# Performance work log

Measured on AMD Instinct MI355X. Metric: run time of the kernel, lower is better.

## Reference

```python
import jax, jax.numpy as jnp
import numpy as np

L = 2048; V = 50000; E = 256
H1 = 512; H2 = 512; H3 = 512; H4 = 512
T = 11; START = 9; STOP = 10; ALPHA = 0.2
NEG = -10000.0


def setup_inputs() -> dict:
    key = jax.random.key(0)
    ks = jax.random.split(key, 25)
    def n(k, shape, s=0.05):
        return jax.random.normal(k, shape, dtype=jnp.float32) * s
    h1 = H1 // 2; h2 = H4 // 2
    trans = jax.random.normal(ks[23], (T, T), dtype=jnp.float32)
    trans = trans.at[START, :].set(NEG).at[:, STOP].set(NEG)
    return {
        "sentence": jax.random.randint(ks[0], (L,), 0, V),
        "emb": n(ks[1], (V, E), 0.1),
        "l1_wih_f": n(ks[2], (4 * h1, E)), "l1_whh_f": n(ks[3], (4 * h1, h1)), "l1_b_f": n(ks[4], (4 * h1,)),
        "l1_wih_b": n(ks[5], (4 * h1, E)), "l1_whh_b": n(ks[6], (4 * h1, h1)), "l1_b_b": n(ks[7], (4 * h1,)),
        "hc1": n(ks[8], (4, h1)),
        "gat1_W": n(ks[9], (H1, H2)), "gat1_a": n(ks[10], (2 * H2,)),
        "gat2_W": n(ks[11], (H2, H3)), "gat2_a": n(ks[12], (2 * H3,)),
        "l2_wih_f": n(ks[13], (4 * h2, H3)), "l2_whh_f": n(ks[14], (4 * h2, h2)), "l2_b_f": n(ks[15], (4 * h2,)),
        "l2_wih_b": n(ks[16], (4 * h2, H3)), "l2_whh_b": n(ks[17], (4 * h2, h2)), "l2_b_b": n(ks[18], (4 * h2,)),
        "hc2": n(ks[19], (4, h2)),
        "w_tag": n(ks[20], (T, H4)), "b_tag": n(ks[21], (T,)),
        "trans": trans,
    }


def _lstm_dir(x, h0, c0, wih, whh, b):
    # x: [L, D]; PyTorch gate order i, f, g, o
    def step(carry, xt):
        h, c = carry
        z = xt @ wih.T + h @ whh.T + b
        i, f, g, o = jnp.split(z, 4)
        i = jax.nn.sigmoid(i); f = jax.nn.sigmoid(f)
        g = jnp.tanh(g); o = jax.nn.sigmoid(o)
        c = f * c + i * g
        h = o * jnp.tanh(c)
        return (h, c), h
    _, hs = jax.lax.scan(step, (h0, c0), x)
    return hs


def _bilstm(x, wf, uf, bf, wb, ub, bb, hc):
    hf = _lstm_dir(x, hc[0], hc[1], wf, uf, bf)
    hb = _lstm_dir(x[::-1], hc[2], hc[3], wb, ub, bb)[::-1]
    return jnp.concatenate([hf, hb], axis=-1)  # [L, 2h]


def _gat(h, W, a):
    # dense GAT layer: attention over all node pairs (inference, no dropout)
    Wh = h @ W                                   # [L, F]
    F = W.shape[1]
    e = jax.nn.leaky_relu((Wh @ a[:F])[:, None] + (Wh @ a[F:])[None, :], ALPHA)  # [L, L]
    attn = jax.nn.softmax(e, axis=1)
    return attn @ Wh


def _viterbi(feats, trans):
    init = jnp.full((T,), NEG, dtype=feats.dtype).at[START].set(0.0)
    def step(fv, feat):
        scores = fv[None, :] + trans             # [next_tag, prev_tag]
        bp = jnp.argmax(scores, axis=1)
        fv2 = jnp.max(scores, axis=1) + feat
        return fv2, bp
    fv, bps = jax.lax.scan(step, init, feats)    # bps: [L, T]
    term = fv + trans[STOP]
    best = jnp.argmax(term)
    score = term[best]
    def back(tag, bp):
        return bp[tag], tag
    _, path = jax.lax.scan(back, best, bps, reverse=True)
    return score, path


def reference(sentence, emb, l1_wih_f, l1_whh_f, l1_b_f, l1_wih_b, l1_whh_b, l1_b_b, hc1,
              gat1_W, gat1_a, gat2_W, gat2_a,
              l2_wih_f, l2_whh_f, l2_b_f, l2_wih_b, l2_whh_b, l2_b_b, hc2,
              w_tag, b_tag, trans):
    x = emb[sentence]                                                  # [L, E]
    h1 = _bilstm(x, l1_wih_f, l1_whh_f, l1_b_f, l1_wih_b, l1_whh_b, l1_b_b, hc1)
    g1 = jax.nn.elu(_gat(h1, gat1_W, gat1_a))
    g2 = jax.nn.elu(_gat(g1, gat2_W, gat2_a))
    h2 = _bilstm(g2, l2_wih_f, l2_whh_f, l2_b_f, l2_wih_b, l2_whh_b, l2_b_b, hc2)
    feats = h2 @ w_tag.T + b_tag                                       # [L, T]
    score, path = _viterbi(feats, trans)
    return score, path
```

## Files before the change

kernel.cpp:

```cpp
#include <hip/hip_runtime.h>
#include <hip/hip_bf16.h>
#include <math.h>

#define SEQL 2048
#define EDIM 256
#define HID 256
#define G4 1024
#define HCAT 512
#define TT 11
#define START_TAG 9
#define STOP_TAG 10
#define NEGV -10000.0f
#define ALPHA_LR 0.2f
#define VCH 64
#define VCS 32
#define NU 16
#define NBLK 16

__device__ __forceinline__ float sigf(float x) { return 1.0f / (1.0f + __expf(-x)); }
__device__ __forceinline__ float tanhfast(float x) { return 2.0f / (1.0f + __expf(-2.0f * x)) - 1.0f; }
__device__ __forceinline__ unsigned int bfp(float f) {
    union { float f; unsigned int u; } c; c.f = f;
    return (c.u + 0x7FFFu + ((c.u >> 16) & 1u)) >> 16;
}
__device__ __forceinline__ float bflo(unsigned int u) { return __uint_as_float(u << 16); }
__device__ __forceinline__ float bfhi(unsigned int u) { return __uint_as_float(u & 0xFFFF0000u); }

__global__ void embed_k(const int* __restrict__ sent, const float* __restrict__ emb,
                        float* __restrict__ x) {
    int idx = blockIdx.x * 256 + threadIdx.x;
    int t = idx >> 8, e = idx & 255;
    x[idx] = emb[(size_t)sent[t] * EDIM + e];
}

__global__ __launch_bounds__(256) void gemm_nt(const float* __restrict__ A,
                                               const float* __restrict__ B,
                                               const float* __restrict__ bias,
                                               float* __restrict__ C,
                                               int M, int N, int K) {
    __shared__ float As[16][68];
    __shared__ float Bs[16][68];
    int tid = threadIdx.x;
    int tx = tid & 15, ty = tid >> 4;
    int m0 = blockIdx.y * 64, n0 = blockIdx.x * 64;
    int lr = tid >> 2;
    int lc = (tid & 3) * 4;
    float acc[4][4] = {};
    for (int k0 = 0; k0 < K; k0 += 16) {
        float4 av = *(const float4*)(A + (size_t)(m0 + lr) * K + k0 + lc);
        float4 bv = make_float4(0.f, 0.f, 0.f, 0.f);
        if (n0 + lr < N) bv = *(const float4*)(B + (size_t)(n0 + lr) * K + k0 + lc);
        As[lc + 0][lr] = av.x; As[lc + 1][lr] = av.y; As[lc + 2][lr] = av.z; As[lc + 3][lr] = av.w;
        Bs[lc + 0][lr] = bv.x; Bs[lc + 1][lr] = bv.y; Bs[lc + 2][lr] = bv.z; Bs[lc + 3][lr] = bv.w;
        __syncthreads();
#pragma unroll
        for (int kk = 0; kk < 16; ++kk) {
            float4 a4 = *(const float4*)&As[kk][ty * 4];
            float4 b4 = *(const float4*)&Bs[kk][tx * 4];
            float aa[4] = {a4.x, a4.y, a4.z, a4.w};
            float bb[4] = {b4.x, b4.y, b4.z, b4.w};
#pragma unroll
            for (int i = 0; i < 4; ++i)
#pragma unroll
                for (int j = 0; j < 4; ++j) acc[i][j] += aa[i] * bb[j];
        }
        __syncthreads();
    }
#pragma unroll
    for (int i = 0; i < 4; ++i) {
        int m = m0 + ty * 4 + i;
#pragma unroll
        for (int j = 0; j < 4; ++j) {
            int n = n0 + tx * 4 + j;
            if (n < N) {
                float v = acc[i][j];
                if (bias) v += bias[n];
                C[(size_t)m * N + n] = v;
            }
        }
    }
}

__global__ __launch_bounds__(256) void gemm_nn_ks(const float* __restrict__ A,
                                                  const float* __restrict__ B,
                                                  float* __restrict__ Cpart,
                                                  int M, int N, int K4) {
    __shared__ float As[16][68];
    __shared__ float Bs[16][68];
    int tid = threadIdx.x;
    int tx = tid & 15, ty = tid >> 4;
    int m0 = blockIdx.y * 64, n0 = blockIdx.x * 64;
    int kz = blockIdx.z;
    int K = (int)gridDim.z * K4;
    int kbeg = kz * K4, kend = kbeg + K4;
    int lr = tid >> 2;
    int lc = (tid & 3) * 4;
    int br = tid >> 4;
    int bc = (tid & 15) * 4;
    float acc[4][4] = {};
    for (int k0 = kbeg; k0 < kend; k0 += 16) {
        float4 av = *(const float4*)(A + (size_t)(m0 + lr) * K + k0 + lc);
        float4 bv = *(const float4*)(B + (size_t)(k0 + br) * N + n0 + bc);
        As[lc + 0][lr] = av.x; As[lc + 1][lr] = av.y; As[lc + 2][lr] = av.z; As[lc + 3][lr] = av.w;
        *(float4*)&Bs[br][bc] = bv;
        __syncthreads();
#pragma unroll
        for (int kk = 0; kk < 16; ++kk) {
            float4 a4 = *(const float4*)&As[kk][ty * 4];
            float4 b4 = *(const float4*)&Bs[kk][tx * 4];
            float aa[4] = {a4.x, a4.y, a4.z, a4.w};
            float bb[4] = {b4.x, b4.y, b4.z, b4.w};
#pragma unroll
            for (int i = 0; i < 4; ++i)
#pragma unroll
                for (int j = 0; j < 4; ++j) acc[i][j] += aa[i] * bb[j];
        }
        __syncthreads();
    }
    float* Cz = Cpart + (size_t)kz * M * N;
#pragma unroll
    for (int i = 0; i < 4; ++i) {
        int m = m0 + ty * 4 + i;
#pragma unroll
        for (int j = 0; j < 4; ++j) {
            int n = n0 + tx * 4 + j;
            Cz[(size_t)m * N + n] = acc[i][j];
        }
    }
}

__global__ void attn_fin(const float* __restrict__ Cp, const float* __restrict__ Zr,
                         float* __restrict__ C, int MN, int N) {
    int idx = blockIdx.x * 256 + threadIdx.x;
    float v = Cp[idx] + Cp[MN + idx] + Cp[2 * MN + idx] + Cp[3 * MN + idx];
    v /= Zr[idx / N];
    C[idx] = v > 0.f ? v : (__expf(v) - 1.f);
}

__global__ void sum4_fin(const float* __restrict__ Cp, float* __restrict__ C, int MN) {
    int idx = blockIdx.x * 256 + threadIdx.x;
    C[idx] = Cp[idx] + Cp[MN + idx] + Cp[2 * MN + idx] + Cp[3 * MN + idx];
}

__global__ __launch_bounds__(256) void lstm_lds(const float* __restrict__ xin_f,
                                                const float* __restrict__ xin_b,
                                                const float* __restrict__ whh_f,
                                                const float* __restrict__ whh_b,
                                                const float* __restrict__ hc,
                                                float* __restrict__ out,
                                                unsigned int* pubu, int tagbase) {
    int raw = blockIdx.x;
    int lane7 = raw & 7;
    if (lane7 > 1) return;
    int dir = lane7;
    int b = raw >> 3;
    const float* xin = dir ? xin_b : xin_f;
    const float* whh = dir ? whh_b : whh_f;

    int tid = threadIdx.x;

    __shared__ uint4 W4[2048];
    __shared__ __align__(16) float hbuf[256];
    __shared__ float zp[512];

    for (int idx = tid; idx < 2048; idx += 256) {
        int wave = idx >> 9;
        int i = (idx >> 6) & 7;
        int l = idx & 63;
        int towner = wave * 64 + l;
        int rp = towner & 31;
        int k8 = towner >> 5;
        int rloc = 2 * rp + (i >> 2);
        int ii = i & 3;
        int g = rloc >> 4, j = rloc & 15;
        const float* wr = whh + (size_t)(g * HID + b * NU + j) * HID + k8 * 32 + ii * 8;
        uint4 v;
        v.x = bfp(wr[0]) | (bfp(wr[1]) << 16);
        v.y = bfp(wr[2]) | (bfp(wr[3]) << 16);
        v.z = bfp(wr[4]) | (bfp(wr[5]) << 16);
        v.w = bfp(wr[6]) | (bfp(wr[7]) << 16);
        W4[wave * 512 + i * 64 + l] = v;
    }

    if (tid < 256) hbuf[tid] = hc[dir * 512 + tid];
    float c = 0.f;
    float xq0 = 0.f, xq1 = 0.f, xq2 = 0.f, xq3 = 0.f;
    if (tid < 16) {
        c = hc[dir * 512 + 256 + b * NU + tid];
        int t0 = dir ? (SEQL - 1) : 0;
        const float* xr = xin + (size_t)t0 * G4 + b * NU + tid;
        xq0 = xr[0]; xq1 = xr[256]; xq2 = xr[512]; xq3 = xr[768];
    }
    __syncthreads();

    int rp = tid & 31;
    int k8 = tid >> 5;
    int wbase = (tid >> 6) * 512 + (tid & 63);
    const float4* hb4 = (const float4*)hbuf;

    int ppair = tid - 64;
    int upair = (ppair < b * 8) ? ppair : ppair + 8;

    for (int s = 0; s < SEQL; ++s) {
        float acc0 = 0.f, acc1 = 0.f;
#pragma unroll
        for (int i = 0; i < 4; ++i) {
            uint4 w0 = W4[wbase + i * 64];
            uint4 w1 = W4[wbase + (i + 4) * 64];
            float4 hA = hb4[k8 * 8 + i * 2];
            float4 hB = hb4[k8 * 8 + i * 2 + 1];
            acc0 += bflo(w0.x) * hA.x + bfhi(w0.x) * hA.y + bflo(w0.y) * hA.z + bfhi(w0.y) * hA.w
                  + bflo(w0.z) * hB.x + bfhi(w0.z) * hB.y + bflo(w0.w) * hB.z + bfhi(w0.w) * hB.w;
            acc1 += bflo(w1.x) * hA.x + bfhi(w1.x) * hA.y + bflo(w1.y) * hA.z + bfhi(w1.y) * hA.w
                  + bflo(w1.z) * hB.x + bfhi(w1.z) * hB.y + bflo(w1.w) * hB.z + bfhi(w1.w) * hB.w;
        }
        zp[k8 * 64 + 2 * rp] = acc0;
        zp[k8 * 64 + 2 * rp + 1] = acc1;
        __syncthreads();

        int t = dir ? (SEQL - 1 - s) : s;
        unsigned int etag = (unsigned int)(tagbase + s + 1) & 0xFFFFu;
        unsigned int* slot = pubu + (((s + 1) & 1) * 2 + dir) * 256;

        if (tid < 16) {
            float zi = xq0, zf = xq1, zg = xq2, zo = xq3;
#pragma unroll
            for (int q = 0; q < 8; ++q) {
                zi += zp[q * 64 + tid];
                zf += zp[q * 64 + 16 + tid];
                zg += zp[q * 64 + 32 + tid];
                zo += zp[q * 64 + 48 + tid];
            }
            float ig = sigf(zi), fg = sigf(zf), gt = tanhfast(zg), og = sigf(zo);
            c = fg * c + ig * gt;
            float hn = og * tanhfast(c);
            hbuf[b * NU + tid] = hn;
            unsigned int word = (bfp(hn) << 16) | etag;
            unsigned int wnext = __shfl_down(word, 1, 64);
            if ((tid & 1) == 0) {
                unsigned long long w64 = (unsigned long long)word |
                                         ((unsigned long long)wnext << 32);
                __hip_atomic_store((unsigned long long*)&slot[b * NU + tid], w64,
                                   __ATOMIC_RELAXED, __HIP_MEMORY_SCOPE_AGENT);
            }
            out[(size_t)t * HCAT + dir * HID + b * NU + tid] = hn;
            if (s + 1 < SEQL) {
                int tn = dir ? (SEQL - 2 - s) : (s + 1);
                const float* xr = xin + (size_t)tn * G4 + b * NU + tid;
                xq0 = xr[0]; xq1 = xr[256]; xq2 = xr[512]; xq3 = xr[768];
            }
        } else if (tid >= 64 && tid < 184 && s + 1 < SEQL) {
            unsigned long long v;
            for (;;) {
                v = __hip_atomic_load((unsigned long long*)&slot[upair * 2],
                                      __ATOMIC_RELAXED, __HIP_MEMORY_SCOPE_AGENT);
                if ((unsigned int)(v & 0xFFFFu) == etag &&
                    (unsigned int)((v >> 32) & 0xFFFFu) == etag) break;
            }
            hbuf[upair * 2]     = bfhi((unsigned int)v);
            hbuf[upair * 2 + 1] = bfhi((unsigned int)(v >> 32));
        }
        __syncthreads();
    }
}

__global__ void gat_scores(const float* __restrict__ Wh, const float* __restrict__ a,
                           float* __restrict__ s1, float* __restrict__ s2) {
    int i = blockIdx.x;
    int lane = threadIdx.x;
    const float* rowp = Wh + (size_t)i * HCAT;
    float p1 = 0.f, p2 = 0.f;
    for (int k = lane; k < HCAT; k += 64) {
        float w = rowp[k];
        p1 += w * a[k];
        p2 += w * a[HCAT + k];
    }
    for (int off = 32; off; off >>= 1) {
        p1 += __shfl_down(p1, off, 64);
        p2 += __shfl_down(p2, off, 64);
    }
    if (lane == 0) { s1[i] = p1; s2[i] = p2; }
}

__global__ void reduce_max_k(const float* __restrict__ s2, float* __restrict__ outv) {
    __shared__ float red[256];
    int tid = threadIdx.x;
    float m = -INFINITY;
    for (int k = tid; k < SEQL; k += 256) m = fmaxf(m, s2[k]);
    red[tid] = m;
    __syncthreads();
    for (int off = 128; off; off >>= 1) {
        if (tid < off) red[tid] = fmaxf(red[tid], red[tid + off]);
        __syncthreads();
    }
    if (tid == 0) outv[0] = red[0];
}

__global__ void gat_p(const float* __restrict__ s1, const float* __restrict__ s2,
                      const float* __restrict__ s2m, float* __restrict__ P,
                      float* __restrict__ Z) {
    int i = blockIdx.x;
    int tid = threadIdx.x;
    float base = s1[i];
    float m = base + s2m[0];
    m = m > 0.f ? m : ALPHA_LR * m;
    float zs = 0.f;
    for (int jj = tid; jj < SEQL; jj += 256) {
        float e = base + s2[jj];
        e = e > 0.f ? e : ALPHA_LR * e;
        float p = __expf(e - m);
        P[(size_t)i * SEQL + jj] = p;
        zs += p;
    }
    __shared__ float red[256];
    red[tid] = zs;
    __syncthreads();
    for (int off = 128; off; off >>= 1) {
        if (tid < off) red[tid] += red[tid + off];
        __syncthreads();
    }
    if (tid == 0) Z[i] = red[0];
}

__global__ void vit_chunkA(const float* __restrict__ feats, const float* __restrict__ trans,
                           float* __restrict__ chunkA) {
    int c = blockIdx.x;
    int tid = threadIdx.x;
    __shared__ float Acur[121], tr[121];
    if (tid < 121) tr[tid] = trans[tid];
    __syncthreads();
    int n = tid / 11, p = tid % 11;
    int t0 = c * VCS;
    if (tid < 121) Acur[tid] = tr[tid] + feats[t0 * TT + n];
    __syncthreads();
    for (int t = t0 + 1; t < t0 + VCS; ++t) {
        float v = -INFINITY;
        if (tid < 121) {
            float ft = feats[t * TT + n];
#pragma unroll
            for (int k = 0; k < 11; ++k) v = fmaxf(v, tr[n * 11 + k] + Acur[k * 11 + p]);
            v += ft;
        }
        __syncthreads();
        if (tid < 121) Acur[tid] = v;
        __syncthreads();
    }
    if (tid < 121) chunkA[c * 121 + tid] = Acur[tid];
}

__global__ void vit_prefix(const float* __restrict__ chunkA, float* __restrict__ fvstart) {
    int tid = threadIdx.x;
    __shared__ float fv[11];
    if (tid < 11) fv[tid] = (tid == START_TAG) ? 0.f : NEGV;
    __syncthreads();
    if (tid < 11) fvstart[tid] = fv[tid];
    for (int c = 0; c < VCH; ++c) {
        float v = -INFINITY;
        if (tid < 11) {
            for (int p = 0; p < 11; ++p) v = fmaxf(v, chunkA[c * 121 + tid * 11 + p] + fv[p]);
        }
        __syncthreads();
        if (tid < 11) { fv[tid] = v; fvstart[(c + 1) * TT + tid] = v; }
        __syncthreads();
    }
}

__global__ void vit_chunkC(const float* __restrict__ feats, const float* __restrict__ trans,
                           const float* __restrict__ fvstart, int* __restrict__ bp,
                           float* __restrict__ fvfinal) {
    int c = blockIdx.x;
    int tid = threadIdx.x;
    __shared__ float fv[11], tr[121], sc[121], mx[11];
    if (tid < 121) tr[tid] = trans[tid];
    if (tid < 11) fv[tid] = fvstart[c * TT + tid];
    __syncthreads();
    int t0 = c * VCS;
    for (int t = t0; t < t0 + VCS; ++t) {
        if (tid < 121) sc[tid] = fv[tid % 11] + tr[tid];
        __syncthreads();
        if (tid < 11) {
            float best = -INFINITY;
            int bi = 0;
            for (int k = 0; k < 11; ++k) {
                float v = sc[tid * 11 + k];
                if (v > best) { best = v; bi = k; }
            }
            bp[t * TT + tid] = bi;
            mx[tid] = best + feats[t * TT + tid];
        }
        __syncthreads();
        if (tid < 11) fv[tid] = mx[tid];
        __syncthreads();
    }
    if (c == VCH - 1 && tid < 11) fvfinal[tid] = fv[tid];
}

__global__ __launch_bounds__(1024) void vit_back(const int* __restrict__ bp,
                                                 const float* __restrict__ fvfinal,
                                                 const float* __restrict__ trans,
                                                 float* __restrict__ outp) {
    __shared__ unsigned char bufA[SEQL * TT];
    __shared__ unsigned char bufB[SEQL * TT];
    __shared__ int bestIdx;
    int tid = threadIdx.x;
    for (int idx = tid; idx < SEQL * TT; idx += 1024) {
        int t = idx / TT, n = idx - t * TT;
        bufA[idx] = (t < SEQL - 1) ? (unsigned char)bp[(t + 1) * TT + n] : (unsigned char)n;
    }
    __syncthreads();
    unsigned char* a = bufA;
    unsigned char* b = bufB;
    for (int len = 1; len < SEQL - 1; len <<= 1) {
        for (int idx = tid; idx < SEQL * TT; idx += 1024) {
            int t = idx / TT, n = idx - t * TT;
            int m = (t + len <= SEQL - 1) ? (int)a[(t + len) * TT + n] : n;
            b[t * TT + n] = a[t * TT + m];
        }
        __syncthreads();
        unsigned char* tmp = a; a = b; b = tmp;
        __syncthreads();
    }
    if (tid == 0) {
        float bs = -INFINITY;
        int bi = 0;
        for (int p = 0; p < 11; ++p) {
            float v = fvfinal[p] + trans[STOP_TAG * 11 + p];
            if (v > bs) { bs = v; bi = p; }
        }
        outp[0] = bs;
        bestIdx = bi;
    }
    __syncthreads();
    int best = bestIdx;
    for (int t = tid; t < SEQL; t += 1024) outp[1 + t] = (float)a[t * TT + best];
}

extern "C" void kernel_launch(void* const* d_in, const int* in_sizes, int n_in,
                              void* d_out, int out_size, void* d_ws, size_t ws_size,
                              hipStream_t stream) {
    const int* sent = (const int*)d_in[0];
    const float* emb = (const float*)d_in[1];
    const float* w1f = (const float*)d_in[2];
    const float* u1f = (const float*)d_in[3];
    const float* b1f = (const float*)d_in[4];
    const float* w1b = (const float*)d_in[5];
    const float* u1b = (const float*)d_in[6];
    const float* b1b = (const float*)d_in[7];
    const float* hc1 = (const float*)d_in[8];
    const float* g1W = (const float*)d_in[9];
    const float* g1a = (const float*)d_in[10];
    const float* g2W = (const float*)d_in[11];
    const float* g2a = (const float*)d_in[12];
    const float* w2f = (const float*)d_in[13];
    const float* u2f = (const float*)d_in[14];
    const float* b2f = (const float*)d_in[15];
    const float* w2b = (const float*)d_in[16];
    const float* u2b = (const float*)d_in[17];
    const float* b2b = (const float*)d_in[18];
    const float* hc2 = (const float*)d_in[19];
    const float* wtag = (const float*)d_in[20];
    const float* btag = (const float*)d_in[21];
    const float* trans = (const float*)d_in[22];

    float* ws = (float*)d_ws;
    float* x = ws;
    float* R1 = x + 524288;
    float* xin_f = R1;
    float* xin_b = R1 + 2097152;
    float* P = R1;
    float* h1cat = R1 + 4194304;
    float* Wh = h1cat + 1048576;
    float* g1 = Wh + 1048576;
    float* s1 = g1 + 1048576;
    float* s2 = s1 + 2048;
    float* Zr = s2 + 2048;
    float* s2m = Zr + 2048;
    unsigned int* pub = (unsigned int*)(s2m + 16);
    float* feats = (float*)(pub + 1024);
    float* chA = feats + 22528;
    float* fvst = chA + 7744;
    float* fvfin = fvst + 720;
    int* bp = (int*)(fvfin + 16);
    float* Cpart = (float*)(bp + 22528);

    hipMemsetAsync(pub, 0, 1024 * sizeof(unsigned int), stream);

    embed_k<<<SEQL, 256, 0, stream>>>(sent, emb, x);

    gemm_nt<<<dim3(16, 32), 256, 0, stream>>>(x, w1f, b1f, xin_f, SEQL, G4, EDIM);
    gemm_nt<<<dim3(16, 32), 256, 0, stream>>>(x, w1b, b1b, xin_b, SEQL, G4, EDIM);
    lstm_lds<<<128, 256, 0, stream>>>(xin_f, xin_b, u1f, u1b, hc1, h1cat, pub, 0);

    gemm_nn_ks<<<dim3(8, 32, 4), 256, 0, stream>>>(h1cat, g1W, Cpart, SEQL, HCAT, HCAT / 4);
    sum4_fin<<<4096, 256, 0, stream>>>(Cpart, Wh, SEQL * HCAT);
    gat_scores<<<SEQL, 64, 0, stream>>>(Wh, g1a, s1, s2);
    reduce_max_k<<<1, 256, 0, stream>>>(s2, s2m);
    gat_p<<<SEQL, 256, 0, stream>>>(s1, s2, s2m, P, Zr);
    gemm_nn_ks<<<dim3(8, 32, 4), 256, 0, stream>>>(P, Wh, Cpart, SEQL, HCAT, SEQL / 4);
    attn_fin<<<4096, 256, 0, stream>>>(Cpart, Zr, g1, SEQL * HCAT, HCAT);

    gemm_nn_ks<<<dim3(8, 32, 4), 256, 0, stream>>>(g1, g2W, Cpart, SEQL, HCAT, HCAT / 4);
    sum4_fin<<<4096, 256, 0, stream>>>(Cpart, Wh, SEQL * HCAT);
    gat_scores<<<SEQL, 64, 0, stream>>>(Wh, g2a, s1, s2);
    reduce_max_k<<<1, 256, 0, stream>>>(s2, s2m);
    gat_p<<<SEQL, 256, 0, stream>>>(s1, s2, s2m, P, Zr);
    float* g2v = h1cat;
    gemm_nn_ks<<<dim3(8, 32, 4), 256, 0, stream>>>(P, Wh, Cpart, SEQL, HCAT, SEQL / 4);
    attn_fin<<<4096, 256, 0, stream>>>(Cpart, Zr, g2v, SEQL * HCAT, HCAT);

    gemm_nt<<<dim3(16, 32), 256, 0, stream>>>(g2v, w2f, b2f, xin_f, SEQL, G4, HCAT);
    gemm_nt<<<dim3(16, 32), 256, 0, stream>>>(g2v, w2b, b2b, xin_b, SEQL, G4, HCAT);
    float* h2cat = g1;
    lstm_lds<<<128, 256, 0, stream>>>(xin_f, xin_b, u2f, u2b, hc2, h2cat, pub, 2048);

    gemm_nt<<<dim3(1, 32), 256, 0, stream>>>(h2cat, wtag, btag, feats, SEQL, TT, HCAT);
    vit_chunkA<<<VCH, 128, 0, stream>>>(feats, trans, chA);
    vit_prefix<<<1, 128, 0, stream>>>(chA, fvst);
    vit_chunkC<<<VCH, 128, 0, stream>>>(feats, trans, fvst, bp, fvfin);
    vit_back<<<1, 1024, 0, stream>>>(bp, fvfin, trans, (float*)d_out);
}
```

Baseline: 6.757 ms.

## Place LSTM blocks per direction on one XCC via runtime census

The LSTM kernel now launches 256 blocks. Each block reads its hardware XCC ID, registers in a global census, and waits at a grid barrier. Each direction's 16 cooperating blocks are then chosen from a single XCC, so the per-step hidden-state exchange stays inside one chiplet's L2. The poll loop now mostly uses volatile loads with a periodic agent-scope atomic, and the producer adds a volatile store. This relies on all 256 blocks being co-resident for the spin barrier, and on volatile loads seeing cross-CU writes within one XCC; either failing risks deadlock or stale reads.

```diff
diff --git a/kernel.cpp b/kernel.cpp
--- a/kernel.cpp
+++ b/kernel.cpp
@@ -148,16 +148,47 @@
                                                 const float* __restrict__ whh_b,
                                                 const float* __restrict__ hc,
                                                 float* __restrict__ out,
-                                                unsigned int* pubu, int tagbase) {
-    int raw = blockIdx.x;
-    int lane7 = raw & 7;
-    if (lane7 > 1) return;
-    int dir = lane7;
-    int b = raw >> 3;
+                                                unsigned int* pubu, int* census,
+                                                int tagbase) {
+    int tid = threadIdx.x;
+    __shared__ int role_s, dirb_s;
+    __shared__ unsigned xcc_s;
+
+    if (tid == 0) {
+        unsigned xcc;
+        asm volatile("s_getreg_b32 %0, hwreg(HW_REG_XCC_ID)" : "=s"(xcc));
+        xcc &= 7u;
+        xcc_s = xcc;
+        role_s = atomicAdd(&census[xcc], 1);
+        atomicAdd(&census[8], 1);
+        while (__hip_atomic_load(&census[8], __ATOMIC_ACQUIRE,
+                                 __HIP_MEMORY_SCOPE_AGENT) < (int)gridDim.x) {}
+        int cnt[8];
+        for (int i = 0; i < 8; ++i)
+            cnt[i] = __hip_atomic_load(&census[i], __ATOMIC_RELAXED,
+                                       __HIP_MEMORY_SCOPE_AGENT);
+        int xA = 0;
+        for (int i = 1; i < 8; ++i) if (cnt[i] > cnt[xA]) xA = i;
+        int xB = (xA == 0) ? 1 : 0;
+        for (int i = 0; i < 8; ++i)
+            if (i != xA && cnt[i] > cnt[xB]) xB = i;
+        int dir = -1, b = -1;
+        int xcb = (int)xcc_s, roleb = role_s;
+        if (xcb == xA && roleb < 16) { dir = 0; b = roleb; }
+        if (cnt[xB] >= 16) {
+            if (xcb == xB && roleb < 16) { dir = 1; b = roleb; }
+        } else {
+            if (xcb == xA && roleb >= 16 && roleb < 32) { dir = 1; b = roleb - 16; }
+        }
+        dirb_s = (dir < 0) ? -1 : (dir * 16 + b);
+    }
+    __syncthreads();
+    if (dirb_s < 0) return;
+    int dir = dirb_s >> 4;
+    int b = dirb_s & 15;
+
     const float* xin = dir ? xin_b : xin_f;
     const float* whh = dir ? whh_b : whh_f;
-
-    int tid = threadIdx.x;
 
     __shared__ uint4 W4[2048];
     __shared__ __align__(16) float hbuf[256];
@@ -240,6 +271,7 @@
             if ((tid & 1) == 0) {
                 unsigned long long w64 = (unsigned long long)word |
                                          ((unsigned long long)wnext << 32);
+                *(volatile unsigned long long*)&slot[b * NU + tid] = w64;
                 __hip_atomic_store((unsigned long long*)&slot[b * NU + tid], w64,
                                    __ATOMIC_RELAXED, __HIP_MEMORY_SCOPE_AGENT);
             }
@@ -250,12 +282,17 @@
                 xq0 = xr[0]; xq1 = xr[256]; xq2 = xr[512]; xq3 = xr[768];
             }
         } else if (tid >= 64 && tid < 184 && s + 1 < SEQL) {
-            unsigned long long v;
+            unsigned long long v; int it = 0;
             for (;;) {
-                v = __hip_atomic_load((unsigned long long*)&slot[upair * 2],
-                                      __ATOMIC_RELAXED, __HIP_MEMORY_SCOPE_AGENT);
+                v = *(volatile const unsigned long long*)&slot[upair * 2];
                 if ((unsigned int)(v & 0xFFFFu) == etag &&
                     (unsigned int)((v >> 32) & 0xFFFFu) == etag) break;
+                if ((++it & 7) == 0) {
+                    v = __hip_atomic_load((unsigned long long*)&slot[upair * 2],
+                                          __ATOMIC_RELAXED, __HIP_MEMORY_SCOPE_AGENT);
+                    if ((unsigned int)(v & 0xFFFFu) == etag &&
+                        (unsigned int)((v >> 32) & 0xFFFFu) == etag) break;
+                }
             }
             hbuf[upair * 2]     = bfhi((unsigned int)v);
             hbuf[upair * 2 + 1] = bfhi((unsigned int)(v >> 32));
@@ -476,20 +513,22 @@
     float* Zr = s2 + 2048;
     float* s2m = Zr + 2048;
     unsigned int* pub = (unsigned int*)(s2m + 16);
-    float* feats = (float*)(pub + 1024);
+    int* census1 = (int*)(pub + 1024);
+    int* census2 = census1 + 16;
+    float* feats = (float*)(census2 + 16);
     float* chA = feats + 22528;
     float* fvst = chA + 7744;
     float* fvfin = fvst + 720;
     int* bp = (int*)(fvfin + 16);
     float* Cpart = (float*)(bp + 22528);
 
-    hipMemsetAsync(pub, 0, 1024 * sizeof(unsigned int), stream);
+    hipMemsetAsync(pub, 0, (1024 + 32) * sizeof(unsigned int), stream);
 
     embed_k<<<SEQL, 256, 0, stream>>>(sent, emb, x);
 
     gemm_nt<<<dim3(16, 32), 256, 0, stream>>>(x, w1f, b1f, xin_f, SEQL, G4, EDIM);
     gemm_nt<<<dim3(16, 32), 256, 0, stream>>>(x, w1b, b1b, xin_b, SEQL, G4, EDIM);
-    lstm_lds<<<128, 256, 0, stream>>>(xin_f, xin_b, u1f, u1b, hc1, h1cat, pub, 0);
+    lstm_lds<<<256, 256, 0, stream>>>(xin_f, xin_b, u1f, u1b, hc1, h1cat, pub, census1, 0);
 
     gemm_nn_ks<<<dim3(8, 32, 4), 256, 0, stream>>>(h1cat, g1W, Cpart, SEQL, HCAT, HCAT / 4);
     sum4_fin<<<4096, 256, 0, stream>>>(Cpart, Wh, SEQL * HCAT);
@@ -511,7 +550,7 @@
     gemm_nt<<<dim3(16, 32), 256, 0, stream>>>(g2v, w2f, b2f, xin_f, SEQL, G4, HCAT);
     gemm_nt<<<dim3(16, 32), 256, 0, stream>>>(g2v, w2b, b2b, xin_b, SEQL, G4, HCAT);
     float* h2cat = g1;
-    lstm_lds<<<128, 256, 0, stream>>>(xin_f, xin_b, u2f, u2b, hc2, h2cat, pub, 2048);
+    lstm_lds<<<256, 256, 0, stream>>>(xin_f, xin_b, u2f, u2b, hc2, h2cat, pub, census2, 2048);
 
     gemm_nt<<<dim3(1, 32), 256, 0, stream>>>(h2cat, wtag, btag, feats, SEQL, TT, HCAT);
     vit_chunkA<<<VCH, 128, 0, stream>>>(feats, trans, chA);
```

Result: slower. 7.554 ms (+11.8%).

## Reduce LSTM partial sums with wave shuffles and pad hidden-state LDS buffer

Applied to the files above, without the earlier changes.

Remaps the LSTM recurrent matvec so the 8 k-slices of each row pair sit on adjacent lanes. The partial sums are then reduced with xor-shuffles inside the wave instead of going through an 8-way LDS scratch reduction done by 16 threads. The hidden-state buffer is padded (36-float stride per 32 entries) to avoid LDS bank conflicts now that lanes in a wave read different k-slices. This shortens the serial per-step critical path, at the cost of extra shuffle instructions and index arithmetic.

```diff
diff --git a/kernel.cpp b/kernel.cpp
--- a/kernel.cpp
+++ b/kernel.cpp
@@ -16,6 +16,7 @@
 #define VCS 32
 #define NU 16
 #define NBLK 16
+#define HIDX(u) ((((u) >> 5) * 36) + ((u) & 31))
 
 __device__ __forceinline__ float sigf(float x) { return 1.0f / (1.0f + __expf(-x)); }
 __device__ __forceinline__ float tanhfast(float x) { return 2.0f / (1.0f + __expf(-2.0f * x)) - 1.0f; }
@@ -160,16 +161,16 @@
     int tid = threadIdx.x;
 
     __shared__ uint4 W4[2048];
-    __shared__ __align__(16) float hbuf[256];
-    __shared__ float zp[512];
+    __shared__ __align__(16) float hbuf[288];
+    __shared__ float zred[64];
 
     for (int idx = tid; idx < 2048; idx += 256) {
         int wave = idx >> 9;
         int i = (idx >> 6) & 7;
         int l = idx & 63;
         int towner = wave * 64 + l;
-        int rp = towner & 31;
-        int k8 = towner >> 5;
+        int rp = towner >> 3;
+        int k8 = towner & 7;
         int rloc = 2 * rp + (i >> 2);
         int ii = i & 3;
         int g = rloc >> 4, j = rloc & 15;
@@ -182,7 +183,7 @@
         W4[wave * 512 + i * 64 + l] = v;
     }
 
-    if (tid < 256) hbuf[tid] = hc[dir * 512 + tid];
+    if (tid < 256) hbuf[HIDX(tid)] = hc[dir * 512 + tid];
     float c = 0.f;
     float xq0 = 0.f, xq1 = 0.f, xq2 = 0.f, xq3 = 0.f;
     if (tid < 16) {
@@ -193,29 +194,34 @@
     }
     __syncthreads();
 
-    int rp = tid & 31;
-    int k8 = tid >> 5;
+    int rp = tid >> 3;
+    int k8 = tid & 7;
     int wbase = (tid >> 6) * 512 + (tid & 63);
-    const float4* hb4 = (const float4*)hbuf;
 
     int ppair = tid - 64;
     int upair = (ppair < b * 8) ? ppair : ppair + 8;
 
     for (int s = 0; s < SEQL; ++s) {
+        const float4* hp = (const float4*)(hbuf + k8 * 36);
         float acc0 = 0.f, acc1 = 0.f;
 #pragma unroll
         for (int i = 0; i < 4; ++i) {
             uint4 w0 = W4[wbase + i * 64];
             uint4 w1 = W4[wbase + (i + 4) * 64];
-            float4 hA = hb4[k8 * 8 + i * 2];
-            float4 hB = hb4[k8 * 8 + i * 2 + 1];
+            float4 hA = hp[i * 2];
+            float4 hB = hp[i * 2 + 1];
             acc0 += bflo(w0.x) * hA.x + bfhi(w0.x) * hA.y + bflo(w0.y) * hA.z + bfhi(w0.y) * hA.w
                   + bflo(w0.z) * hB.x + bfhi(w0.z) * hB.y + bflo(w0.w) * hB.z + bfhi(w0.w) * hB.w;
             acc1 += bflo(w1.x) * hA.x + bfhi(w1.x) * hA.y + bflo(w1.y) * hA.z + bfhi(w1.y) * hA.w
                   + bflo(w1.z) * hB.x + bfhi(w1.z) * hB.y + bflo(w1.w) * hB.z + bfhi(w1.w) * hB.w;
         }
-        zp[k8 * 64 + 2 * rp] = acc0;
-        zp[k8 * 64 + 2 * rp + 1] = acc1;
+        acc0 += __shfl_xor(acc0, 1, 64); acc1 += __shfl_xor(acc1, 1, 64);
+        acc0 += __shfl_xor(acc0, 2, 64); acc1 += __shfl_xor(acc1, 2, 64);
+        acc0 += __shfl_xor(acc0, 4, 64); acc1 += __shfl_xor(acc1, 4, 64);
+        if (k8 == 0) {
+            zred[2 * rp] = acc0;
+            zred[2 * rp + 1] = acc1;
+        }
         __syncthreads();
 
         int t = dir ? (SEQL - 1 - s) : s;
@@ -223,27 +229,24 @@
         unsigned int* slot = pubu + (((s + 1) & 1) * 2 + dir) * 256;
 
         if (tid < 16) {
-            float zi = xq0, zf = xq1, zg = xq2, zo = xq3;
-#pragma unroll
-            for (int q = 0; q < 8; ++q) {
-                zi += zp[q * 64 + tid];
-                zf += zp[q * 64 + 16 + tid];
-                zg += zp[q * 64 + 32 + tid];
-                zo += zp[q * 64 + 48 + tid];
-            }
+            float zi = xq0 + zred[tid];
+            float zf = xq1 + zred[16 + tid];
+            float zg = xq2 + zred[32 + tid];
+            float zo = xq3 + zred[48 + tid];
             float ig = sigf(zi), fg = sigf(zf), gt = tanhfast(zg), og = sigf(zo);
             c = fg * c + ig * gt;
             float hn = og * tanhfast(c);
-            hbuf[b * NU + tid] = hn;
+            int u = b * NU + tid;
+            hbuf[HIDX(u)] = hn;
             unsigned int word = (bfp(hn) << 16) | etag;
             unsigned int wnext = __shfl_down(word, 1, 64);
             if ((tid & 1) == 0) {
                 unsigned long long w64 = (unsigned long long)word |
                                          ((unsigned long long)wnext << 32);
-                __hip_atomic_store((unsigned long long*)&slot[b * NU + tid], w64,
+                __hip_atomic_store((unsigned long long*)&slot[u], w64,
                                    __ATOMIC_RELAXED, __HIP_MEMORY_SCOPE_AGENT);
             }
-            out[(size_t)t * HCAT + dir * HID + b * NU + tid] = hn;
+            out[(size_t)t * HCAT + dir * HID + u] = hn;
             if (s + 1 < SEQL) {
                 int tn = dir ? (SEQL - 2 - s) : (s + 1);
                 const float* xr = xin + (size_t)tn * G4 + b * NU + tid;
@@ -257,8 +260,8 @@
                 if ((unsigned int)(v & 0xFFFFu) == etag &&
                     (unsigned int)((v >> 32) & 0xFFFFu) == etag) break;
             }
-            hbuf[upair * 2]     = bfhi((unsigned int)v);
-            hbuf[upair * 2 + 1] = bfhi((unsigned int)(v >> 32));
+            hbuf[HIDX(upair * 2)]     = bfhi((unsigned int)v);
+            hbuf[HIDX(upair * 2 + 1)] = bfhi((unsigned int)(v >> 32));
         }
         __syncthreads();
     }
```

Result: faster. 6.508 ms (-3.7%).
